# Optimization experiments

Hardware: AMD Instinct MI355X
Metric: run time of the kernel (lower is better)

The kernel has to match this reference:

```python
import jax, jax.numpy as jnp
import numpy as np

T, N_ROI, B, HID = 16, 32, 16, 768
NUM_NODES = T * N_ROI  # 512


def build_temporal_edges(T, N):
    # frame-internal fully-connected (includes self loops), then adjacent-frame same-ROI
    nodes = np.arange(T * N, dtype=np.int32).reshape(T, N)
    src_intra = np.repeat(nodes, N, axis=1).reshape(-1)
    dst_intra = np.tile(nodes, (1, N)).reshape(-1)
    a = nodes[:-1].reshape(-1)
    b = nodes[1:].reshape(-1)
    src = np.concatenate([src_intra, a, b])
    dst = np.concatenate([dst_intra, b, a])
    return jnp.asarray(src), jnp.asarray(dst)


def gat_layer(x, W, att_src, att_dst, bias, src, dst, concat):
    # x: (num_nodes, in_dim); W: (in_dim, H*C)
    H, C = att_src.shape
    n = x.shape[0]
    h = (x @ W).reshape(n, H, C)
    a_s = (h * att_src[None]).sum(-1)  # (n, H)
    a_d = (h * att_dst[None]).sum(-1)  # (n, H)
    e = jax.nn.leaky_relu(a_s[src] + a_d[dst], negative_slope=0.2)  # (E, H)
    e_max = jax.ops.segment_max(e, dst, num_segments=n)
    ex = jnp.exp(e - e_max[dst])
    denom = jax.ops.segment_sum(ex, dst, num_segments=n)
    alpha = ex / (denom[dst] + 1e-16)  # per-destination softmax (PyG semantics)
    msg = h[src] * alpha[:, :, None]  # (E, H, C)
    out = jax.ops.segment_sum(msg, dst, num_segments=n)  # (n, H, C)
    out = out.reshape(n, H * C) if concat else out.mean(axis=1)
    return out + bias


def setup_inputs() -> dict:
    key = jax.random.key(0)
    ks = jax.random.split(key, 14)
    s = lambda k, shape, fan: jax.random.normal(k, shape, jnp.float32) * (1.0 / np.sqrt(fan))
    edge_src, edge_dst = build_temporal_edges(T, N_ROI)
    return {
        "node_feats": jax.random.normal(ks[0], (B, NUM_NODES, HID), jnp.float32),
        "W1": s(ks[1], (HID, 512), HID),
        "att_src1": s(ks[2], (4, 128), 128),
        "att_dst1": s(ks[3], (4, 128), 128),
        "b1": jnp.zeros((512,), jnp.float32),
        "W2": s(ks[4], (512, 128), 512),
        "att_src2": s(ks[5], (1, 128), 128),
        "att_dst2": s(ks[6], (1, 128), 128),
        "b2": jnp.zeros((128,), jnp.float32),
        "fc_w": s(ks[7], (128, HID), 128),
        "fc_b": jnp.zeros((HID,), jnp.float32),
        "cls_w": s(ks[8], (HID, 2), HID),
        "cls_b": jnp.zeros((2,), jnp.float32),
        "edge_src": edge_src,
        "edge_dst": edge_dst,
    }


def reference(node_feats, W1, att_src1, att_dst1, b1, W2, att_src2, att_dst2, b2,
              fc_w, fc_b, cls_w, cls_b, edge_src, edge_dst):
    def one_graph(x):
        x = jax.nn.elu(gat_layer(x, W1, att_src1, att_dst1, b1, edge_src, edge_dst, True))
        x = jax.nn.elu(gat_layer(x, W2, att_src2, att_dst2, b2, edge_src, edge_dst, False))
        g = x.mean(axis=0)              # mean pool over T*N nodes -> (128,)
        emb = g @ fc_w + fc_b           # (768,)
        return emb @ cls_w + cls_b      # (num_classes,)
    return jax.vmap(one_graph)(node_feats)  # (B, num_classes)
```

## Files before the change

### kernel.cpp

```cpp
#include <hip/hip_runtime.h>
#include <hip/hip_bf16.h>
#include <math.h>

#define TT 16
#define NROI 32
#define BB 16
#define HID 768
#define NODES 512
#define MROWS (BB * NODES)
#define D1 512
#define D2 128

typedef __attribute__((ext_vector_type(8))) short short8;
typedef __attribute__((ext_vector_type(4))) float f32x4;

__device__ __forceinline__ void bf16_split(float v, short& h, short& l) {
    unsigned u = __float_as_uint(v);
    h = (short)(u >> 16);
    float r = v - __uint_as_float(u & 0xFFFF0000u);
    l = (short)(__float_as_uint(r) >> 16);
}

__device__ __forceinline__ float lrelu02(float v) { return v > 0.0f ? v : 0.2f * v; }

#define XBLKS (MROWS * HID / 2048)
__launch_bounds__(256)
__global__ void prep_kernel(const float* __restrict__ X, short* __restrict__ xh,
                            short* __restrict__ xl,
                            const float* __restrict__ W1, short* __restrict__ w1h,
                            short* __restrict__ w1l, const float* __restrict__ W2,
                            short* __restrict__ w2h, short* __restrict__ w2l,
                            const float* __restrict__ fc_w, const float* __restrict__ fc_b,
                            const float* __restrict__ cls_w, const float* __restrict__ cls_b,
                            float* __restrict__ fw, float* __restrict__ fb) {
    const int bid = blockIdx.x;
    const int tid = threadIdx.x;

    if (bid < XBLKS) {
        const size_t i0 = (size_t)bid * 2048 + tid * 8;
        float4 v0 = *(const float4*)(X + i0);
        float4 v1 = *(const float4*)(X + i0 + 4);
        float vv[8] = {v0.x, v0.y, v0.z, v0.w, v1.x, v1.y, v1.z, v1.w};
        short8 h8, l8;
#pragma unroll
        for (int j = 0; j < 8; ++j) {
            short h, l;
            bf16_split(vv[j], h, l);
            h8[j] = h; l8[j] = l;
        }
        *(short8*)(xh + i0) = h8;
        *(short8*)(xl + i0) = l8;
        return;
    }

    if (bid < XBLKS + 112) {
        __shared__ unsigned tile[64][65];
        const float* W; short *hi, *lo; int K, N, k0, n0;
        int tb = bid - XBLKS;
        if (tb < 96) {
            W = W1; hi = w1h; lo = w1l; K = HID; N = D1;
            k0 = (tb >> 3) * 64; n0 = (tb & 7) * 64;
        } else {
            int idx = tb - 96;
            W = W2; hi = w2h; lo = w2l; K = D1; N = D2;
            k0 = (idx >> 1) * 64; n0 = (idx & 1) * 64;
        }
#pragma unroll
        for (int it = 0; it < 16; ++it) {
            int i = it * 256 + tid;
            int r = i >> 6, j = i & 63;
            float v = W[(size_t)(k0 + r) * N + n0 + j];
            short h, l;
            bf16_split(v, h, l);
            tile[r][j] = ((unsigned)(unsigned short)h << 16) | (unsigned)(unsigned short)l;
        }
        __syncthreads();
#pragma unroll
        for (int it = 0; it < 16; ++it) {
            int i = it * 256 + tid;
            int rr = i >> 6, c = i & 63;
            unsigned p = tile[c][rr];
            hi[(size_t)(n0 + rr) * K + k0 + c] = (short)(p >> 16);
            lo[(size_t)(n0 + rr) * K + k0 + c] = (short)(p & 0xFFFF);
        }
        return;
    }

    const int t = tid;
    const int c = t >> 1, j = t & 1;
    const float* wr = fc_w + (size_t)c * HID;
    float s = 0.0f;
#pragma unroll 4
    for (int o = 0; o < HID; o += 4) {
        float4 w4 = *(const float4*)(wr + o);
        s += w4.x * cls_w[(o + 0) * 2 + j] + w4.y * cls_w[(o + 1) * 2 + j]
           + w4.z * cls_w[(o + 2) * 2 + j] + w4.w * cls_w[(o + 3) * 2 + j];
    }
    fw[c * 2 + j] = s;

    __shared__ float p0[256], p1[256];
    float a0 = 0.0f, a1 = 0.0f;
    for (int o = t * 3; o < t * 3 + 3; ++o) {
        float v = fc_b[o];
        a0 += v * cls_w[o * 2 + 0];
        a1 += v * cls_w[o * 2 + 1];
    }
    p0[t] = a0; p1[t] = a1;
    __syncthreads();
    for (int off = 128; off > 0; off >>= 1) {
        if (t < off) { p0[t] += p0[t + off]; p1[t] += p1[t + off]; }
        __syncthreads();
    }
    if (t == 0) { fb[0] = p0[0] + cls_b[0]; fb[1] = p1[0] + cls_b[1]; }
}

template <int PROJ>
__launch_bounds__(256)
__global__ void gemm_ps_kernel(const short* __restrict__ Ah, const short* __restrict__ Al,
                               const short* __restrict__ Bh, const short* __restrict__ Bl,
                               float* __restrict__ C,
                               const float* __restrict__ asw, const float* __restrict__ adw,
                               float* __restrict__ as_o, float* __restrict__ ad_o,
                               int N, int K) {
    constexpr int BM = 64, BN = 128, BK = 32, LD = BK + 8;
    __shared__ __align__(16) short As[2][2][BM][LD];
    __shared__ __align__(16) short Bs[2][2][BN][LD];
    __shared__ float eps[2][BM], epd[2][BM];

    const int tid = threadIdx.x, lane = tid & 63, wid = tid >> 6;
    const int brow = blockIdx.y * BM, bcol = blockIdx.x * BN;
    const int wm = (wid >> 1) * 32, wn = (wid & 1) * 64;
    const int frow = lane & 15, fk = (lane >> 4) * 8;

    f32x4 acc[2][4];
#pragma unroll
    for (int m = 0; m < 2; ++m)
#pragma unroll
        for (int n = 0; n < 4; ++n) acc[m][n] = (f32x4)0.0f;

    short8 a_h, a_l, b_h[2], b_l[2];
    const int arow = tid >> 2, ag = tid & 3;

    auto load_tiles = [&](int k0) {
        const size_t aoff = (size_t)(brow + arow) * K + k0 + ag * 8;
        a_h = *(const short8*)(Ah + aoff);
        a_l = *(const short8*)(Al + aoff);
#pragma unroll
        for (int it = 0; it < 2; ++it) {
            int idx = it * 256 + tid;
            int row = idx >> 2, g = idx & 3;
            const size_t boff = (size_t)(bcol + row) * K + k0 + g * 8;
            b_h[it] = *(const short8*)(Bh + boff);
            b_l[it] = *(const short8*)(Bl + boff);
        }
    };
    auto write_tiles = [&](int buf) {
        *(short8*)&As[buf][0][arow][ag * 8] = a_h;
        *(short8*)&As[buf][1][arow][ag * 8] = a_l;
#pragma unroll
        for (int it = 0; it < 2; ++it) {
            int idx = it * 256 + tid;
            int row = idx >> 2, g = idx & 3;
            *(short8*)&Bs[buf][0][row][g * 8] = b_h[it];
            *(short8*)&Bs[buf][1][row][g * 8] = b_l[it];
        }
    };

    const int NT = K / BK;
    load_tiles(0);
    write_tiles(0);
    __syncthreads();
    int cur = 0;
    for (int t = 0; t < NT; ++t) {
        if (t + 1 < NT) load_tiles((t + 1) * BK);

        short8 ah[2], al[2], bhf[4], blf[4];
#pragma unroll
        for (int m = 0; m < 2; ++m) {
            ah[m] = *(const short8*)&As[cur][0][wm + m * 16 + frow][fk];
            al[m] = *(const short8*)&As[cur][1][wm + m * 16 + frow][fk];
        }
#pragma unroll
        for (int n = 0; n < 4; ++n) {
            bhf[n] = *(const short8*)&Bs[cur][0][wn + n * 16 + frow][fk];
            blf[n] = *(const short8*)&Bs[cur][1][wn + n * 16 + frow][fk];
        }
#pragma unroll
        for (int m = 0; m < 2; ++m)
#pragma unroll
            for (int n = 0; n < 4; ++n) {
                acc[m][n] = __builtin_amdgcn_mfma_f32_16x16x32_bf16(ah[m], bhf[n], acc[m][n], 0, 0, 0);
                acc[m][n] = __builtin_amdgcn_mfma_f32_16x16x32_bf16(ah[m], blf[n], acc[m][n], 0, 0, 0);
                acc[m][n] = __builtin_amdgcn_mfma_f32_16x16x32_bf16(al[m], bhf[n], acc[m][n], 0, 0, 0);
            }

        if (t + 1 < NT) write_tiles(cur ^ 1);
        __syncthreads();
        cur ^= 1;
    }

#pragma unroll
    for (int m = 0; m < 2; ++m)
#pragma unroll
        for (int n = 0; n < 4; ++n) {
            const int col = bcol + wn + n * 16 + (lane & 15);
            const int r0 = brow + wm + m * 16 + (lane >> 4) * 4;
#pragma unroll
            for (int j = 0; j < 4; ++j)
                C[(size_t)(r0 + j) * N + col] = acc[m][n][j];
        }

    if constexpr (PROJ > 0) {
        const int hh = (PROJ == 4) ? (int)blockIdx.x : 0;
        float aw[4], dw[4];
#pragma unroll
        for (int n = 0; n < 4; ++n) {
            int c = wn + n * 16 + (lane & 15);
            aw[n] = asw[hh * 128 + c];
            dw[n] = adw[hh * 128 + c];
        }
        float ps[2][4], pd[2][4];
#pragma unroll
        for (int m = 0; m < 2; ++m)
#pragma unroll
            for (int j = 0; j < 4; ++j) {
                float s = 0.0f, d = 0.0f;
#pragma unroll
                for (int n = 0; n < 4; ++n) {
                    s += acc[m][n][j] * aw[n];
                    d += acc[m][n][j] * dw[n];
                }
                ps[m][j] = s; pd[m][j] = d;
            }
#pragma unroll
        for (int off = 1; off < 16; off <<= 1)
#pragma unroll
            for (int m = 0; m < 2; ++m)
#pragma unroll
                for (int j = 0; j < 4; ++j) {
                    ps[m][j] += __shfl_xor(ps[m][j], off);
                    pd[m][j] += __shfl_xor(pd[m][j], off);
                }
        if ((lane & 15) == 0) {
#pragma unroll
            for (int m = 0; m < 2; ++m)
#pragma unroll
                for (int j = 0; j < 4; ++j) {
                    int rl = wm + m * 16 + (lane >> 4) * 4 + j;
                    eps[wid & 1][rl] = ps[m][j];
                    epd[wid & 1][rl] = pd[m][j];
                }
        }
        __syncthreads();
        if (tid < BM) {
            float s = eps[0][tid] + eps[1][tid];
            float d = epd[0][tid] + epd[1][tid];
            if (PROJ == 4) {
                as_o[(size_t)(brow + tid) * 4 + hh] = s;
                ad_o[(size_t)(brow + tid) * 4 + hh] = d;
            } else {
                as_o[brow + tid] = s;
                ad_o[brow + tid] = d;
            }
        }
    }
}

__device__ __forceinline__ void softmax_rows(const float* sas, const float* sad,
                                             const float* sasm, const float* sasp,
                                             float (*sal)[36], int t, int tid) {
    if (tid < 128) {
        const int r = tid >> 2, p = tid & 3;
        const float ad = sad[r];
        float e[8];
        float m = -1e30f;
#pragma unroll
        for (int k = 0; k < 8; ++k) {
            e[k] = lrelu02(sas[p * 8 + k] + ad);
            m = fmaxf(m, e[k]);
        }
        m = fmaxf(m, __shfl_xor(m, 1));
        m = fmaxf(m, __shfl_xor(m, 2));
        const bool hp = (t > 0), hn = (t < TT - 1);
        float vp = 0.0f, vn = 0.0f;
        if (hp) { vp = lrelu02(sasm[r] + ad); m = fmaxf(m, vp); }
        if (hn) { vn = lrelu02(sasp[r] + ad); m = fmaxf(m, vn); }
        float sum = 0.0f;
#pragma unroll
        for (int k = 0; k < 8; ++k) {
            float x = expf(e[k] - m);
            e[k] = x;
            sum += x;
        }
        sum += __shfl_xor(sum, 1);
        sum += __shfl_xor(sum, 2);
        float ep = hp ? expf(vp - m) : 0.0f;
        float en = hn ? expf(vn - m) : 0.0f;
        sum += ep + en;
        float inv = 1.0f / (sum + 1e-16f);
#pragma unroll
        for (int k = 0; k < 8; ++k) sal[r][p * 8 + k] = e[k] * inv;
        if (p == 0) { sal[r][32] = ep * inv; sal[r][33] = en * inv; }
    }
}

__launch_bounds__(256)
__global__ void edge_agg1_kernel(const float* __restrict__ h1, const float* __restrict__ a_s,
                                 const float* __restrict__ a_d, const float* __restrict__ b1,
                                 short* __restrict__ x1h, short* __restrict__ x1l) {
    const int bid = blockIdx.x;
    const int hh = bid & 3;
    const int bt = bid >> 2;
    const int b = bt >> 4;
    const int t = bt & 15;
    const int tid = threadIdx.x;
    __shared__ float sh[NROI * 128];
    __shared__ float sal[NROI][36];
    __shared__ float sas[NROI], sad[NROI], sasm[NROI], sasp[NROI];

    const int base = b * NODES + t * NROI;
    const float* src = h1 + (size_t)base * D1 + hh * 128;
#pragma unroll
    for (int it = 0; it < 4; ++it) {
        int i = it * 256 + tid;
        int row = i >> 5, c4 = i & 31;
        *(float4*)&sh[row * 128 + c4 * 4] = *(const float4*)&src[(size_t)row * D1 + c4 * 4];
    }
    if (tid < NROI) {
        sas[tid] = a_s[(base + tid) * 4 + hh];
        sad[tid] = a_d[(base + tid) * 4 + hh];
        sasm[tid] = (t > 0) ? a_s[(base - NROI + tid) * 4 + hh] : 0.0f;
        sasp[tid] = (t < TT - 1) ? a_s[(base + NROI + tid) * 4 + hh] : 0.0f;
    }
    __syncthreads();

    softmax_rows(sas, sad, sasm, sasp, sal, t, tid);
    __syncthreads();

    const float* hprev = h1 + (size_t)(base - NROI) * D1 + hh * 128;
    const float* hnext = h1 + (size_t)(base + NROI) * D1 + hh * 128;
    short* outh = x1h + (size_t)base * D1 + hh * 128;
    short* outl = x1l + (size_t)base * D1 + hh * 128;

    const int g = tid >> 5;
    const int ch0 = (tid & 31) * 4;
    const float4 bb = *(const float4*)&b1[hh * 128 + ch0];

    f32x4 acc[4];
#pragma unroll
    for (int rr = 0; rr < 4; ++rr) acc[rr] = (f32x4)0.0f;

#pragma unroll
    for (int sb = 0; sb < NROI; sb += 4) {
        f32x4 a0 = *(const f32x4*)&sal[g][sb];
        f32x4 a1 = *(const f32x4*)&sal[g + 8][sb];
        f32x4 a2 = *(const f32x4*)&sal[g + 16][sb];
        f32x4 a3 = *(const f32x4*)&sal[g + 24][sb];
#pragma unroll
        for (int k = 0; k < 4; ++k) {
            f32x4 v = *(const f32x4*)&sh[(sb + k) * 128 + ch0];
            acc[0] += a0[k] * v;
            acc[1] += a1[k] * v;
            acc[2] += a2[k] * v;
            acc[3] += a3[k] * v;
        }
    }

#pragma unroll
    for (int rr = 0; rr < 4; ++rr) {
        const int r = g + rr * 8;
        f32x4 a = acc[rr];
        if (t > 0) {
            f32x4 v = *(const f32x4*)&hprev[(size_t)r * D1 + ch0];
            a += sal[r][32] * v;
        }
        if (t < TT - 1) {
            f32x4 v = *(const f32x4*)&hnext[(size_t)r * D1 + ch0];
            a += sal[r][33] * v;
        }
        a[0] += bb.x; a[1] += bb.y; a[2] += bb.z; a[3] += bb.w;
#pragma unroll
        for (int k = 0; k < 4; ++k) a[k] = a[k] > 0.f ? a[k] : expf(a[k]) - 1.f;
        short4 h4, l4;
        bf16_split(a[0], h4.x, l4.x);
        bf16_split(a[1], h4.y, l4.y);
        bf16_split(a[2], h4.z, l4.z);
        bf16_split(a[3], h4.w, l4.w);
        *(short4*)&outh[(size_t)r * D1 + ch0] = h4;
        *(short4*)&outl[(size_t)r * D1 + ch0] = l4;
    }
}

__launch_bounds__(256)
__global__ void edge_agg2_pool_kernel(const float* __restrict__ h2, const float* __restrict__ a_s,
                                      const float* __restrict__ a_d, const float* __restrict__ b2,
                                      float* __restrict__ pg) {
    const int bid = blockIdx.x;
    const int q = bid & 3;
    const int bt = bid >> 2;
    const int b = bt >> 4;
    const int t = bt & 15;
    const int tid = threadIdx.x;
    __shared__ float sh[NROI * 32];
    __shared__ float sal[NROI][36];
    __shared__ float sas[NROI], sad[NROI], sasm[NROI], sasp[NROI];
    __shared__ float red[NROI][8][4];
    __shared__ float red2[8][8][4];

    const int base = b * NODES + t * NROI;
    const float* src = h2 + (size_t)base * D2 + q * 32;
    {
        int row = tid >> 3, c4 = tid & 7;
        *(float4*)&sh[row * 32 + c4 * 4] = *(const float4*)&src[(size_t)row * D2 + c4 * 4];
    }
    if (tid < NROI) {
        sas[tid] = a_s[base + tid];
        sad[tid] = a_d[base + tid];
        sasm[tid] = (t > 0) ? a_s[base - NROI + tid] : 0.0f;
        sasp[tid] = (t < TT - 1) ? a_s[base + NROI + tid] : 0.0f;
    }
    __syncthreads();

    softmax_rows(sas, sad, sasm, sasp, sal, t, tid);
    __syncthreads();

    const float* hprev = h2 + (size_t)(base - NROI) * D2 + q * 32;
    const float* hnext = h2 + (size_t)(base + NROI) * D2 + q * 32;

    {
        const int r = tid >> 3, chq = tid & 7;
        const int ch0 = chq * 4;
        const float4 bb = *(const float4*)&b2[q * 32 + ch0];
        f32x4 acc = (f32x4)0.0f;
#pragma unroll
        for (int sb = 0; sb < NROI; sb += 4) {
            f32x4 a4 = *(const f32x4*)&sal[r][sb];
#pragma unroll
            for (int k = 0; k < 4; ++k) {
                f32x4 v = *(const f32x4*)&sh[(sb + k) * 32 + ch0];
                acc += a4[k] * v;
            }
        }
        if (t > 0) {
            f32x4 v = *(const f32x4*)&hprev[(size_t)r * D2 + ch0];
            acc += sal[r][32] * v;
        }
        if (t < TT - 1) {
            f32x4 v = *(const f32x4*)&hnext[(size_t)r * D2 + ch0];
            acc += sal[r][33] * v;
        }
        acc[0] += bb.x; acc[1] += bb.y; acc[2] += bb.z; acc[3] += bb.w;
#pragma unroll
        for (int k = 0; k < 4; ++k) acc[k] = acc[k] > 0.f ? acc[k] : expf(acc[k]) - 1.f;
        *(f32x4*)&red[r][chq][0] = acc;
    }
    __syncthreads();
    if (tid < 64) {
        const int seg = tid >> 3, chq = tid & 7;
        float4 s = make_float4(0.f, 0.f, 0.f, 0.f);
#pragma unroll
        for (int rr = seg * 4; rr < seg * 4 + 4; ++rr) {
            float4 v = *(const float4*)&red[rr][chq][0];
            s.x += v.x; s.y += v.y; s.z += v.z; s.w += v.w;
        }
        *(float4*)&red2[seg][chq][0] = s;
    }
    __syncthreads();
    if (tid < 8) {
        float4 s = make_float4(0.f, 0.f, 0.f, 0.f);
#pragma unroll
        for (int seg = 0; seg < 8; ++seg) {
            float4 v = *(const float4*)&red2[seg][tid][0];
            s.x += v.x; s.y += v.y; s.z += v.z; s.w += v.w;
        }
        *(float4*)&pg[(size_t)bt * D2 + q * 32 + tid * 4] = s;
    }
}

__launch_bounds__(128)
__global__ void pool_cls_kernel(const float* __restrict__ pg, const float* __restrict__ fw,
                                const float* __restrict__ fb, float* __restrict__ out) {
    const int b = blockIdx.x;
    const int tid = threadIdx.x;
    __shared__ float sg[D2];
    float s = 0.0f;
#pragma unroll
    for (int t = 0; t < TT; ++t) s += pg[(size_t)(b * TT + t) * D2 + tid];
    sg[tid] = s;
    __syncthreads();
    const int lane = tid & 63, w = tid >> 6;
    float p = sg[lane] * fw[lane * 2 + w] + sg[lane + 64] * fw[(lane + 64) * 2 + w];
#pragma unroll
    for (int off = 32; off > 0; off >>= 1) p += __shfl_down(p, off);
    if (lane == 0) out[b * 2 + w] = p * (1.0f / (float)NODES) + fb[w];
}

extern "C" void kernel_launch(void* const* d_in, const int* in_sizes, int n_in,
                              void* d_out, int out_size, void* d_ws, size_t ws_size,
                              hipStream_t stream) {
    const float* X        = (const float*)d_in[0];
    const float* W1       = (const float*)d_in[1];
    const float* att_src1 = (const float*)d_in[2];
    const float* att_dst1 = (const float*)d_in[3];
    const float* b1       = (const float*)d_in[4];
    const float* W2       = (const float*)d_in[5];
    const float* att_src2 = (const float*)d_in[6];
    const float* att_dst2 = (const float*)d_in[7];
    const float* b2       = (const float*)d_in[8];
    const float* fc_w     = (const float*)d_in[9];
    const float* fc_b     = (const float*)d_in[10];
    const float* cls_w    = (const float*)d_in[11];
    const float* cls_b    = (const float*)d_in[12];
    float* out = (float*)d_out;

    float* ws = (float*)d_ws;
    float* h1  = ws;
    float* as1 = ws + 4 * 1024 * 1024;
    float* ad1 = as1 + MROWS * 4;
    float* as2 = ad1 + MROWS * 4;
    float* ad2 = as2 + MROWS;
    float* pg  = ad2 + MROWS;
    float* fw  = pg + BB * TT * D2;
    float* fb  = fw + 256;
    short* x1h = (short*)(ws + 5 * 1024 * 1024);
    short* x1l = x1h + (size_t)MROWS * D1;
    short* w1h = (short*)(ws + 9 * 1024 * 1024);
    short* w1l = w1h + D1 * HID;
    short* w2h = w1l + D1 * HID;
    short* w2l = w2h + D2 * D1;
    short* xh  = (short*)(ws + 12 * 1024 * 1024);
    short* xl  = xh + (size_t)MROWS * HID;
    float* h2  = h1;

    prep_kernel<<<XBLKS + 113, 256, 0, stream>>>(X, xh, xl, W1, w1h, w1l, W2, w2h, w2l,
                                                 fc_w, fc_b, cls_w, cls_b, fw, fb);
    gemm_ps_kernel<4><<<dim3(D1 / 128, MROWS / 64), 256, 0, stream>>>(
        xh, xl, w1h, w1l, h1, att_src1, att_dst1, as1, ad1, D1, HID);
    edge_agg1_kernel<<<BB * TT * 4, 256, 0, stream>>>(h1, as1, ad1, b1, x1h, x1l);
    gemm_ps_kernel<1><<<dim3(D2 / 128, MROWS / 64), 256, 0, stream>>>(
        x1h, x1l, w2h, w2l, h2, att_src2, att_dst2, as2, ad2, D2, D1);
    edge_agg2_pool_kernel<<<BB * TT * 4, 256, 0, stream>>>(h2, as2, ad2, b2, pg);
    pool_cls_kernel<<<BB, 128, 0, stream>>>(pg, fw, fb, out);
}
```

Baseline: 103.9 us.

## Store layer-1 activations in bf16 and drop A-low split in second GEMM

The first GEMM now writes h1 as rounded bf16 instead of fp32, and edge_agg1 reads bf16 and emits a single bf16 x1 instead of a hi/lo split. The second GEMM drops the A-low operand, which removes one of its three MFMAs per tile and halves its A loads. The prep kernel also processes four chunks per block with fewer blocks. Together these cut memory traffic on the intermediates, at the cost of lower precision in the hidden activations.

```diff
diff --git a/kernel.cpp b/kernel.cpp
--- a/kernel.cpp
+++ b/kernel.cpp
@@ -21,9 +21,18 @@
     l = (short)(__float_as_uint(r) >> 16);
 }
 
+__device__ __forceinline__ short bf16_rne(float v) {
+    unsigned u = __float_as_uint(v);
+    unsigned r = u + 0x7FFF + ((u >> 16) & 1);
+    return (short)(r >> 16);
+}
+__device__ __forceinline__ float bf16_f32(short s) {
+    return __uint_as_float(((unsigned)(unsigned short)s) << 16);
+}
+
 __device__ __forceinline__ float lrelu02(float v) { return v > 0.0f ? v : 0.2f * v; }
 
-#define XBLKS (MROWS * HID / 2048)
+#define XB2 768
 __launch_bounds__(256)
 __global__ void prep_kernel(const float* __restrict__ X, short* __restrict__ xh,
                             short* __restrict__ xl,
@@ -36,27 +45,30 @@
     const int bid = blockIdx.x;
     const int tid = threadIdx.x;
 
-    if (bid < XBLKS) {
-        const size_t i0 = (size_t)bid * 2048 + tid * 8;
-        float4 v0 = *(const float4*)(X + i0);
-        float4 v1 = *(const float4*)(X + i0 + 4);
-        float vv[8] = {v0.x, v0.y, v0.z, v0.w, v1.x, v1.y, v1.z, v1.w};
-        short8 h8, l8;
-#pragma unroll
-        for (int j = 0; j < 8; ++j) {
-            short h, l;
-            bf16_split(vv[j], h, l);
-            h8[j] = h; l8[j] = l;
-        }
-        *(short8*)(xh + i0) = h8;
-        *(short8*)(xl + i0) = l8;
+    if (bid < XB2) {
+#pragma unroll
+        for (int c = 0; c < 4; ++c) {
+            const size_t i0 = ((size_t)bid * 4 + c) * 2048 + tid * 8;
+            float4 v0 = *(const float4*)(X + i0);
+            float4 v1 = *(const float4*)(X + i0 + 4);
+            float vv[8] = {v0.x, v0.y, v0.z, v0.w, v1.x, v1.y, v1.z, v1.w};
+            short8 h8, l8;
+#pragma unroll
+            for (int j = 0; j < 8; ++j) {
+                short h, l;
+                bf16_split(vv[j], h, l);
+                h8[j] = h; l8[j] = l;
+            }
+            *(short8*)(xh + i0) = h8;
+            *(short8*)(xl + i0) = l8;
+        }
         return;
     }
 
-    if (bid < XBLKS + 112) {
+    if (bid < XB2 + 112) {
         __shared__ unsigned tile[64][65];
         const float* W; short *hi, *lo; int K, N, k0, n0;
-        int tb = bid - XBLKS;
+        int tb = bid - XB2;
         if (tb < 96) {
             W = W1; hi = w1h; lo = w1l; K = HID; N = D1;
             k0 = (tb >> 3) * 64; n0 = (tb & 7) * 64;
@@ -114,16 +126,17 @@
     if (t == 0) { fb[0] = p0[0] + cls_b[0]; fb[1] = p1[0] + cls_b[1]; }
 }
 
-template <int PROJ>
+template <int PROJ, bool ASPLIT, bool CBF16>
 __launch_bounds__(256)
 __global__ void gemm_ps_kernel(const short* __restrict__ Ah, const short* __restrict__ Al,
                                const short* __restrict__ Bh, const short* __restrict__ Bl,
-                               float* __restrict__ C,
+                               void* __restrict__ Cv,
                                const float* __restrict__ asw, const float* __restrict__ adw,
                                float* __restrict__ as_o, float* __restrict__ ad_o,
                                int N, int K) {
     constexpr int BM = 64, BN = 128, BK = 32, LD = BK + 8;
-    __shared__ __align__(16) short As[2][2][BM][LD];
+    constexpr int AP = ASPLIT ? 2 : 1;
+    __shared__ __align__(16) short As[2][AP][BM][LD];
     __shared__ __align__(16) short Bs[2][2][BN][LD];
     __shared__ float eps[2][BM], epd[2][BM];
 
@@ -144,7 +157,7 @@
     auto load_tiles = [&](int k0) {
         const size_t aoff = (size_t)(brow + arow) * K + k0 + ag * 8;
         a_h = *(const short8*)(Ah + aoff);
-        a_l = *(const short8*)(Al + aoff);
+        if constexpr (ASPLIT) a_l = *(const short8*)(Al + aoff);
 #pragma unroll
         for (int it = 0; it < 2; ++it) {
             int idx = it * 256 + tid;
@@ -156,7 +169,7 @@
     };
     auto write_tiles = [&](int buf) {
         *(short8*)&As[buf][0][arow][ag * 8] = a_h;
-        *(short8*)&As[buf][1][arow][ag * 8] = a_l;
+        if constexpr (ASPLIT) *(short8*)&As[buf][1][arow][ag * 8] = a_l;
 #pragma unroll
         for (int it = 0; it < 2; ++it) {
             int idx = it * 256 + tid;
@@ -178,7 +191,7 @@
 #pragma unroll
         for (int m = 0; m < 2; ++m) {
             ah[m] = *(const short8*)&As[cur][0][wm + m * 16 + frow][fk];
-            al[m] = *(const short8*)&As[cur][1][wm + m * 16 + frow][fk];
+            if constexpr (ASPLIT) al[m] = *(const short8*)&As[cur][1][wm + m * 16 + frow][fk];
         }
 #pragma unroll
         for (int n = 0; n < 4; ++n) {
@@ -191,7 +204,8 @@
             for (int n = 0; n < 4; ++n) {
                 acc[m][n] = __builtin_amdgcn_mfma_f32_16x16x32_bf16(ah[m], bhf[n], acc[m][n], 0, 0, 0);
                 acc[m][n] = __builtin_amdgcn_mfma_f32_16x16x32_bf16(ah[m], blf[n], acc[m][n], 0, 0, 0);
-                acc[m][n] = __builtin_amdgcn_mfma_f32_16x16x32_bf16(al[m], bhf[n], acc[m][n], 0, 0, 0);
+                if constexpr (ASPLIT)
+                    acc[m][n] = __builtin_amdgcn_mfma_f32_16x16x32_bf16(al[m], bhf[n], acc[m][n], 0, 0, 0);
             }
 
         if (t + 1 < NT) write_tiles(cur ^ 1);
@@ -206,8 +220,12 @@
             const int col = bcol + wn + n * 16 + (lane & 15);
             const int r0 = brow + wm + m * 16 + (lane >> 4) * 4;
 #pragma unroll
-            for (int j = 0; j < 4; ++j)
-                C[(size_t)(r0 + j) * N + col] = acc[m][n][j];
+            for (int j = 0; j < 4; ++j) {
+                if constexpr (CBF16)
+                    ((short*)Cv)[(size_t)(r0 + j) * N + col] = bf16_rne(acc[m][n][j]);
+                else
+                    ((float*)Cv)[(size_t)(r0 + j) * N + col] = acc[m][n][j];
+            }
         }
 
     if constexpr (PROJ > 0) {
@@ -305,9 +323,9 @@
 }
 
 __launch_bounds__(256)
-__global__ void edge_agg1_kernel(const float* __restrict__ h1, const float* __restrict__ a_s,
+__global__ void edge_agg1_kernel(const short* __restrict__ h1b, const float* __restrict__ a_s,
                                  const float* __restrict__ a_d, const float* __restrict__ b1,
-                                 short* __restrict__ x1h, short* __restrict__ x1l) {
+                                 short* __restrict__ x1b) {
     const int bid = blockIdx.x;
     const int hh = bid & 3;
     const int bt = bid >> 2;
@@ -319,12 +337,15 @@
     __shared__ float sas[NROI], sad[NROI], sasm[NROI], sasp[NROI];
 
     const int base = b * NODES + t * NROI;
-    const float* src = h1 + (size_t)base * D1 + hh * 128;
-#pragma unroll
-    for (int it = 0; it < 4; ++it) {
+    const short* src = h1b + (size_t)base * D1 + hh * 128;
+#pragma unroll
+    for (int it = 0; it < 2; ++it) {
         int i = it * 256 + tid;
-        int row = i >> 5, c4 = i & 31;
-        *(float4*)&sh[row * 128 + c4 * 4] = *(const float4*)&src[(size_t)row * D1 + c4 * 4];
+        int row = i >> 4, c8 = (i & 15) * 8;
+        short8 v = *(const short8*)&src[(size_t)row * D1 + c8];
+        float* dst = &sh[row * 128 + c8];
+#pragma unroll
+        for (int j = 0; j < 8; ++j) dst[j] = bf16_f32(v[j]);
     }
     if (tid < NROI) {
         sas[tid] = a_s[(base + tid) * 4 + hh];
@@ -337,10 +358,9 @@
     softmax_rows(sas, sad, sasm, sasp, sal, t, tid);
     __syncthreads();
 
-    const float* hprev = h1 + (size_t)(base - NROI) * D1 + hh * 128;
-    const float* hnext = h1 + (size_t)(base + NROI) * D1 + hh * 128;
-    short* outh = x1h + (size_t)base * D1 + hh * 128;
-    short* outl = x1l + (size_t)base * D1 + hh * 128;
+    const short* hprev = h1b + (size_t)(base - NROI) * D1 + hh * 128;
+    const short* hnext = h1b + (size_t)(base + NROI) * D1 + hh * 128;
+    short* outp = x1b + (size_t)base * D1 + hh * 128;
 
     const int g = tid >> 5;
     const int ch0 = (tid & 31) * 4;
@@ -371,23 +391,24 @@
         const int r = g + rr * 8;
         f32x4 a = acc[rr];
         if (t > 0) {
-            f32x4 v = *(const f32x4*)&hprev[(size_t)r * D1 + ch0];
-            a += sal[r][32] * v;
+            short4 v4 = *(const short4*)&hprev[(size_t)r * D1 + ch0];
+            float w = sal[r][32];
+            a[0] += w * bf16_f32(v4.x); a[1] += w * bf16_f32(v4.y);
+            a[2] += w * bf16_f32(v4.z); a[3] += w * bf16_f32(v4.w);
         }
         if (t < TT - 1) {
-            f32x4 v = *(const f32x4*)&hnext[(size_t)r * D1 + ch0];
-            a += sal[r][33] * v;
+            short4 v4 = *(const short4*)&hnext[(size_t)r * D1 + ch0];
+            float w = sal[r][33];
+            a[0] += w * bf16_f32(v4.x); a[1] += w * bf16_f32(v4.y);
+            a[2] += w * bf16_f32(v4.z); a[3] += w * bf16_f32(v4.w);
         }
         a[0] += bb.x; a[1] += bb.y; a[2] += bb.z; a[3] += bb.w;
 #pragma unroll
         for (int k = 0; k < 4; ++k) a[k] = a[k] > 0.f ? a[k] : expf(a[k]) - 1.f;
-        short4 h4, l4;
-        bf16_split(a[0], h4.x, l4.x);
-        bf16_split(a[1], h4.y, l4.y);
-        bf16_split(a[2], h4.z, l4.z);
-        bf16_split(a[3], h4.w, l4.w);
-        *(short4*)&outh[(size_t)r * D1 + ch0] = h4;
-        *(short4*)&outl[(size_t)r * D1 + ch0] = l4;
+        short4 o;
+        o.x = bf16_rne(a[0]); o.y = bf16_rne(a[1]);
+        o.z = bf16_rne(a[2]); o.w = bf16_rne(a[3]);
+        *(short4*)&outp[(size_t)r * D1 + ch0] = o;
     }
 }
 
@@ -456,14 +477,14 @@
     }
     __syncthreads();
     if (tid < 64) {
-        const int seg = tid >> 3, chq = tid & 7;
+        const int seg = tid >> 3, cq = tid & 7;
         float4 s = make_float4(0.f, 0.f, 0.f, 0.f);
 #pragma unroll
         for (int rr = seg * 4; rr < seg * 4 + 4; ++rr) {
-            float4 v = *(const float4*)&red[rr][chq][0];
+            float4 v = *(const float4*)&red[rr][cq][0];
             s.x += v.x; s.y += v.y; s.z += v.z; s.w += v.w;
         }
-        *(float4*)&red2[seg][chq][0] = s;
+        *(float4*)&red2[seg][cq][0] = s;
     }
     __syncthreads();
     if (tid < 8) {
@@ -514,31 +535,30 @@
     float* out = (float*)d_out;
 
     float* ws = (float*)d_ws;
-    float* h1  = ws;
-    float* as1 = ws + 4 * 1024 * 1024;
+    short* h1b = (short*)ws;
+    float* h2  = ws + 2 * 1024 * 1024;
+    float* as1 = ws + 3 * 1024 * 1024;
     float* ad1 = as1 + MROWS * 4;
     float* as2 = ad1 + MROWS * 4;
     float* ad2 = as2 + MROWS;
     float* pg  = ad2 + MROWS;
     float* fw  = pg + BB * TT * D2;
     float* fb  = fw + 256;
-    short* x1h = (short*)(ws + 5 * 1024 * 1024);
-    short* x1l = x1h + (size_t)MROWS * D1;
-    short* w1h = (short*)(ws + 9 * 1024 * 1024);
+    short* x1b = (short*)(ws + 4 * 1024 * 1024);
+    short* w1h = (short*)(ws + 6 * 1024 * 1024);
     short* w1l = w1h + D1 * HID;
     short* w2h = w1l + D1 * HID;
     short* w2l = w2h + D2 * D1;
-    short* xh  = (short*)(ws + 12 * 1024 * 1024);
+    short* xh  = (short*)(ws + 8 * 1024 * 1024);
     short* xl  = xh + (size_t)MROWS * HID;
-    float* h2  = h1;
-
-    prep_kernel<<<XBLKS + 113, 256, 0, stream>>>(X, xh, xl, W1, w1h, w1l, W2, w2h, w2l,
-                                                 fc_w, fc_b, cls_w, cls_b, fw, fb);
-    gemm_ps_kernel<4><<<dim3(D1 / 128, MROWS / 64), 256, 0, stream>>>(
-        xh, xl, w1h, w1l, h1, att_src1, att_dst1, as1, ad1, D1, HID);
-    edge_agg1_kernel<<<BB * TT * 4, 256, 0, stream>>>(h1, as1, ad1, b1, x1h, x1l);
-    gemm_ps_kernel<1><<<dim3(D2 / 128, MROWS / 64), 256, 0, stream>>>(
-        x1h, x1l, w2h, w2l, h2, att_src2, att_dst2, as2, ad2, D2, D1);
+
+    prep_kernel<<<XB2 + 113, 256, 0, stream>>>(X, xh, xl, W1, w1h, w1l, W2, w2h, w2l,
+                                               fc_w, fc_b, cls_w, cls_b, fw, fb);
+    gemm_ps_kernel<4, true, true><<<dim3(D1 / 128, MROWS / 64), 256, 0, stream>>>(
+        xh, xl, w1h, w1l, h1b, att_src1, att_dst1, as1, ad1, D1, HID);
+    edge_agg1_kernel<<<BB * TT * 4, 256, 0, stream>>>(h1b, as1, ad1, b1, x1b);
+    gemm_ps_kernel<1, false, false><<<dim3(D2 / 128, MROWS / 64), 256, 0, stream>>>(
+        x1b, nullptr, w2h, w2l, h2, att_src2, att_dst2, as2, ad2, D2, D1);
     edge_agg2_pool_kernel<<<BB * TT * 4, 256, 0, stream>>>(h2, as2, ad2, b2, pg);
     pool_cls_kernel<<<BB, 128, 0, stream>>>(pg, fw, fb, out);
 }
```

Result: faster. 99.88 us (-3.9%).
